# Optimization experiments

Measured on AMD Instinct MI355X. Metric: run time of the kernel, lower is better.

## Reference

```python
import jax, jax.numpy as jnp
import numpy as np

N_PEP, N_MHC, N_TCR = 20000, 5000, 100000
EMB, HID = 128, 256
E_PM, E_MT = 200000, 400000
B = 50000


def setup_inputs() -> dict:
    key = jax.random.key(0)
    ks = jax.random.split(key, 30)
    f32 = jnp.float32

    def w(k, shape, fan_in):
        # torch Linear default: U(-1/sqrt(fan_in), 1/sqrt(fan_in))
        lim = 1.0 / np.sqrt(fan_in)
        return jax.random.uniform(k, shape, dtype=f32, minval=-lim, maxval=lim)

    inp = {
        # embedding tables (learned params)
        "emb_pep": jax.random.normal(ks[0], (N_PEP, EMB), dtype=f32),
        "emb_mhc": jax.random.normal(ks[1], (N_MHC, EMB), dtype=f32),
        "emb_tcr": jax.random.normal(ks[2], (N_TCR, EMB), dtype=f32),
        # edge lists (src=edge_index[0], dst=edge_index[1])
        "src_pm": jax.random.randint(ks[3], (E_PM,), 0, N_PEP, dtype=jnp.int32),
        "dst_pm": jax.random.randint(ks[4], (E_PM,), 0, N_MHC, dtype=jnp.int32),
        "src_mt": jax.random.randint(ks[5], (E_MT,), 0, N_MHC, dtype=jnp.int32),
        "dst_mt": jax.random.randint(ks[6], (E_MT,), 0, N_TCR, dtype=jnp.int32),
        # triplet pack indices
        "pack_pep": jax.random.randint(ks[7], (B,), 0, N_PEP, dtype=jnp.int32),
        "pack_mhc": jax.random.randint(ks[8], (B,), 0, N_MHC, dtype=jnp.int32),
        "pack_tcr": jax.random.randint(ks[9], (B,), 0, N_TCR, dtype=jnp.int32),
        # SAGEConv params: Wl (aggregated neighbors, with bias), Wr (root, no bias)
        # layer 1: pep->mhc (src 128, dst 128); mhc->tcr (src 128, dst 128)
        "l1_pm_Wl": w(ks[10], (HID, EMB), EMB), "l1_pm_bl": w(ks[11], (HID,), EMB),
        "l1_pm_Wr": w(ks[12], (HID, EMB), EMB),
        "l1_mt_Wl": w(ks[13], (HID, EMB), EMB), "l1_mt_bl": w(ks[14], (HID,), EMB),
        "l1_mt_Wr": w(ks[15], (HID, EMB), EMB),
        # layer 2: pep->mhc (src 128, dst 256); mhc->tcr (src 256, dst 256)
        "l2_pm_Wl": w(ks[16], (HID, EMB), EMB), "l2_pm_bl": w(ks[17], (HID,), EMB),
        "l2_pm_Wr": w(ks[18], (HID, HID), HID),
        "l2_mt_Wl": w(ks[19], (HID, HID), HID), "l2_mt_bl": w(ks[20], (HID,), HID),
        "l2_mt_Wr": w(ks[21], (HID, HID), HID),
        # proj_pep and head MLP
        "proj_W": w(ks[22], (HID, EMB), EMB), "proj_b": w(ks[23], (HID,), EMB),
        "head_W1": w(ks[24], (HID, 3 * HID), 3 * HID), "head_b1": w(ks[25], (HID,), 3 * HID),
        "head_W2": w(ks[26], (1, HID), HID), "head_b2": w(ks[27], (1,), HID),
    }
    return inp


def _sage(x_src, x_dst, src, dst, Wl, bl, Wr, n_dst):
    # SAGEConv(mean): lin_l(mean_{j in N(i)} x_src[j]) + lin_r(x_dst[i])
    msg = jax.ops.segment_sum(x_src[src], dst, num_segments=n_dst)  # [n_dst, d_src]
    cnt = jax.ops.segment_sum(jnp.ones((src.shape[0],), x_src.dtype), dst, num_segments=n_dst)
    mean = msg / jnp.maximum(cnt, 1.0)[:, None]
    return mean @ Wl.T + bl + x_dst @ Wr.T


def reference(emb_pep, emb_mhc, emb_tcr,
              src_pm, dst_pm, src_mt, dst_mt,
              pack_pep, pack_mhc, pack_tcr,
              l1_pm_Wl, l1_pm_bl, l1_pm_Wr, l1_mt_Wl, l1_mt_bl, l1_mt_Wr,
              l2_pm_Wl, l2_pm_bl, l2_pm_Wr, l2_mt_Wl, l2_mt_bl, l2_mt_Wr,
              proj_W, proj_b, head_W1, head_b1, head_W2, head_b2):
    relu = jax.nn.relu
    # layer 1 (HeteroConv reads all relations from the same input dict)
    mhc1 = relu(_sage(emb_pep, emb_mhc, src_pm, dst_pm, l1_pm_Wl, l1_pm_bl, l1_pm_Wr, N_MHC))
    tcr1 = relu(_sage(emb_mhc, emb_tcr, src_mt, dst_mt, l1_mt_Wl, l1_mt_bl, l1_mt_Wr, N_TCR))
    # layer 2 ('pep' is never a destination, so it keeps its embedding)
    mhc2 = relu(_sage(emb_pep, mhc1, src_pm, dst_pm, l2_pm_Wl, l2_pm_bl, l2_pm_Wr, N_MHC))
    tcr2 = relu(_sage(mhc1, tcr1, src_mt, dst_mt, l2_mt_Wl, l2_mt_bl, l2_mt_Wr, N_TCR))
    # projections + triplet gather (dropout disabled: inference)
    hp = (emb_pep @ proj_W.T + proj_b)[pack_pep]  # [B, HID]
    hm = mhc2[pack_mhc]
    ht = tcr2[pack_tcr]
    z = jnp.concatenate([hp, hm, ht], axis=-1)  # [B, 3*HID]
    hidden = relu(z @ head_W1.T + head_b1)
    logits = hidden @ head_W2.T + head_b2
    return logits.squeeze(-1)
```

## Files before the change

### kernel.cpp

```cpp
#include <hip/hip_runtime.h>

constexpr int NPEP = 20000, NMHC = 5000, NTCR = 100000;
constexpr int EPM = 200000, EMT = 400000, BB = 50000;
constexpr int MAXU = 50000;

typedef __attribute__((ext_vector_type(8))) short bf16x8;
typedef __attribute__((ext_vector_type(4))) float f32x4;

__device__ inline ushort f2bf(float x) {
    union { float f; unsigned u; } v; v.f = x;
    unsigned r = (v.u + 0x7FFF + ((v.u >> 16) & 1)) >> 16;
    return (ushort)r;
}
__device__ inline float bf2f(ushort b) {
    union { unsigned u; float f; } t; t.u = ((unsigned)b) << 16; return t.f;
}
__device__ inline void bf2x2(unsigned u, float& a, float& b) {
    union { unsigned x; float f; } t1, t2;
    t1.x = u << 16; t2.x = u & 0xffff0000u;
    a = t1.f; b = t2.f;
}
__device__ inline ushort4 f4bf(float4 v) {
    return make_ushort4(f2bf(v.x), f2bf(v.y), f2bf(v.z), f2bf(v.w));
}

constexpr int RS  = 40;
constexpr int RS1 = 136;
constexpr int RS2 = 264;

template <int K, bool HASB, bool AF32>
__device__ void out_tile(ushort* Als, ushort* Wls, int tid, int bx, int by, int M,
                         const void* __restrict__ Av, const ushort* __restrict__ W,
                         const float* __restrict__ bias, ushort* __restrict__ out) {
    const int m0 = bx * 128, n0 = by * 128;
    const int lane = tid & 63, w = tid >> 6;
    const int wm = w >> 1, wn = w & 1;
    const int m16 = lane & 15, q = lane >> 4;

    f32x4 acc[4][4] = {};

    for (int k0 = 0; k0 < K; k0 += 32) {
        bf16x8 a_st[2], w_st[2];
#pragma unroll
        for (int r = 0; r < 2; r++) {
            int chunk = tid + r * 256;
            int row = chunk >> 2, off = (chunk & 3) * 8;
            int ga = min(m0 + row, M - 1);
            if constexpr (AF32) {
                const float* Af = (const float*)Av;
                float4 f0 = *(const float4*)(Af + (size_t)ga * K + k0 + off);
                float4 f1 = *(const float4*)(Af + (size_t)ga * K + k0 + off + 4);
                ushort4 u0 = f4bf(f0), u1 = f4bf(f1);
                bf16x8 av;
                av[0] = (short)u0.x; av[1] = (short)u0.y; av[2] = (short)u0.z; av[3] = (short)u0.w;
                av[4] = (short)u1.x; av[5] = (short)u1.y; av[6] = (short)u1.z; av[7] = (short)u1.w;
                a_st[r] = av;
            } else {
                a_st[r] = *(const bf16x8*)((const ushort*)Av + (size_t)ga * K + k0 + off);
            }
            w_st[r] = *(const bf16x8*)(W + (size_t)(n0 + row) * K + k0 + off);
        }
        __syncthreads();
#pragma unroll
        for (int r = 0; r < 2; r++) {
            int chunk = tid + r * 256;
            int row = chunk >> 2, off = (chunk & 3) * 8;
            *(bf16x8*)(&Als[row * RS + off]) = a_st[r];
            *(bf16x8*)(&Wls[row * RS + off]) = w_st[r];
        }
        __syncthreads();
        bf16x8 af[4], bf[4];
#pragma unroll
        for (int t = 0; t < 4; t++) {
            af[t] = *(const bf16x8*)(&Als[(wm * 64 + t * 16 + m16) * RS + q * 8]);
            bf[t] = *(const bf16x8*)(&Wls[(wn * 64 + t * 16 + m16) * RS + q * 8]);
        }
#pragma unroll
        for (int mt = 0; mt < 4; mt++)
#pragma unroll
            for (int nt = 0; nt < 4; nt++)
                acc[mt][nt] = __builtin_amdgcn_mfma_f32_16x16x32_bf16(af[mt], bf[nt], acc[mt][nt], 0, 0, 0);
    }

#pragma unroll
    for (int mt = 0; mt < 4; mt++) {
#pragma unroll
        for (int i = 0; i < 4; i++) {
            int row = m0 + wm * 64 + mt * 16 + q * 4 + i;
            if (row >= M) continue;
#pragma unroll
            for (int nt = 0; nt < 4; nt++) {
                int col = n0 + wn * 64 + nt * 16 + m16;
                float v = acc[mt][nt][i];
                if (HASB) v += bias[col];
                out[(size_t)row * 256 + col] = f2bf(v);
            }
        }
    }
}

__global__ __launch_bounds__(256) void prep_kernel(
    int* __restrict__ ibz,
    const float4* __restrict__ Wr1f, ushort4* __restrict__ Wr1_b,
    const float4* __restrict__ Wr2f, ushort4* __restrict__ Wr2_b,
    const float* __restrict__ head_W1, ushort4* __restrict__ W1b_b, ushort4* __restrict__ W1c_b,
    const float* __restrict__ l1_pm_Wl, const float* __restrict__ l1_pm_Wr,
    const float* __restrict__ l1_mt_Wl, ushort* __restrict__ Wcat1_b,
    const float* __restrict__ l2_pm_Wl, const float* __restrict__ l2_pm_Wr,
    const float* __restrict__ l2_mt_Wl, ushort* __restrict__ Wcat2_b,
    const float4* __restrict__ emb_mhc, ushort* __restrict__ Acat1,
    const float* __restrict__ proj_W, const float* __restrict__ proj_b,
    ushort* __restrict__ Wcomp_b, float* __restrict__ bp) {
    __shared__ float red[128];
    const int b = blockIdx.x, tid = threadIdx.x;
    if (b < 303) {
        int i = b * 256 + tid;
        if (i < 77500) ((int4*)ibz)[i] = make_int4(0, 0, 0, 0);
    } else if (b < 335) {
        int i = (b - 303) * 256 + tid;
        if (i < 8192) Wr1_b[i] = f4bf(Wr1f[i]);
    } else if (b < 399) {
        int i = (b - 335) * 256 + tid;
        if (i < 16384) Wr2_b[i] = f4bf(Wr2f[i]);
    } else if (b < 463) {
        int i = (b - 399) * 256 + tid;
        if (i < 16384) {
            int n = i >> 6, k4 = (i & 63) * 4;
            W1b_b[i] = f4bf(*(const float4*)(head_W1 + (size_t)n * 768 + 256 + k4));
        }
    } else if (b < 527) {
        int i = (b - 463) * 256 + tid;
        if (i < 16384) {
            int n = i >> 6, k4 = (i & 63) * 4;
            W1c_b[i] = f4bf(*(const float4*)(head_W1 + (size_t)n * 768 + 512 + k4));
        }
    } else if (b < 1039) {
        int idx = (b - 527) * 256 + tid;
        if (idx < 131072) {
            int r = idx >> 8, k = idx & 255;
            float v;
            if (r < 256) v = (k < 128) ? l1_pm_Wl[r * 128 + k] : l1_pm_Wr[r * 128 + (k - 128)];
            else         v = (k < 128) ? 0.f : l1_mt_Wl[(r - 256) * 128 + (k - 128)];
            Wcat1_b[idx] = f2bf(v);
        }
    } else if (b < 1807) {
        int idx = (b - 1039) * 256 + tid;
        if (idx < 196608) {
            int r = idx / 384, k = idx - r * 384;
            float v;
            if (r < 256) v = (k < 128) ? l2_pm_Wl[r * 128 + k] : l2_pm_Wr[r * 256 + (k - 128)];
            else         v = (k < 128) ? 0.f : l2_mt_Wl[(r - 256) * 256 + (k - 128)];
            Wcat2_b[idx] = f2bf(v);
        }
    } else if (b < 2432) {
        int i4 = (b - 1807) * 256 + tid;
        if (i4 < 160000) {
            int r = i4 >> 5, c4 = (i4 & 31) * 4;
            *(ushort4*)(Acat1 + (size_t)r * 256 + 128 + c4) = f4bf(emb_mhc[i4]);
        }
    } else {
        int i = b - 2432;
        const float* w1row = head_W1 + (size_t)i * 768;
        if (tid < 128) {
            float acc = 0.f;
            for (int k = 0; k < 256; k++) acc += w1row[k] * proj_W[k * 128 + tid];
            Wcomp_b[i * 128 + tid] = f2bf(acc);
            red[tid] = w1row[2 * tid] * proj_b[2 * tid] + w1row[2 * tid + 1] * proj_b[2 * tid + 1];
        }
        __syncthreads();
        if (tid < 64) { red[tid] += red[tid + 64]; }
        __syncthreads();
        if (tid < 32) { red[tid] += red[tid + 32]; }
        __syncthreads();
        if (tid == 0) {
            float s = 0.f;
            for (int j = 0; j < 32; j++) s += red[j];
            bp[i] = s;
        }
    }
}

__global__ void hist2_kernel(const int* __restrict__ dst_pm, const int* __restrict__ dst_mt,
                             const int* __restrict__ pack_tcr,
                             int* __restrict__ deg_pm, int* __restrict__ deg_mt,
                             int* __restrict__ mark) {
    int t = blockIdx.x * blockDim.x + threadIdx.x;
    if (t < EPM) atomicAdd(&deg_pm[dst_pm[t]], 1);
    else if (t < EPM + EMT) atomicAdd(&deg_mt[dst_mt[t - EPM]], 1);
    else if (t < EPM + EMT + BB) mark[pack_tcr[t - EPM - EMT]] = 1;
}

__global__ __launch_bounds__(256) void blocksum2_kernel(const int* __restrict__ deg_pm,
                                                        const int* __restrict__ deg_mt,
                                                        const int* __restrict__ mark,
                                                        int* __restrict__ bsum_pm,
                                                        int* __restrict__ bsum_mt,
                                                        int* __restrict__ bsum_mk) {
    __shared__ int red[256];
    const int tid = threadIdx.x;
    const int* deg; int n, bi; int* bsum;
    if (blockIdx.x < 5) { deg = deg_pm; n = NMHC; bi = blockIdx.x; bsum = bsum_pm; }
    else if (blockIdx.x < 103) { deg = deg_mt; n = NTCR; bi = blockIdx.x - 5; bsum = bsum_mt; }
    else { deg = mark; n = NTCR; bi = blockIdx.x - 103; bsum = bsum_mk; }
    const int base = bi * 1024;
    int s = 0;
#pragma unroll
    for (int j = 0; j < 4; j++) {
        int i = base + tid + j * 256;
        if (i < n) s += deg[i];
    }
    red[tid] = s;
    __syncthreads();
    for (int off = 128; off > 0; off >>= 1) {
        if (tid < off) red[tid] += red[tid + off];
        __syncthreads();
    }
    if (tid == 0) bsum[bi] = red[0];
}

__global__ __launch_bounds__(128) void scanb2_kernel(int* __restrict__ bsum_pm,
                                                     int* __restrict__ bsum_mt,
                                                     int* __restrict__ bsum_mk) {
    __shared__ int s[128];
    const int tid = threadIdx.x;
    int* bsum = (blockIdx.x == 0) ? bsum_pm : ((blockIdx.x == 1) ? bsum_mt : bsum_mk);
    const int nb = (blockIdx.x == 0) ? 5 : 98;
    int v = (tid < nb) ? bsum[tid] : 0;
    s[tid] = v;
    __syncthreads();
    for (int off = 1; off < 128; off <<= 1) {
        int t = (tid >= off) ? s[tid - off] : 0;
        __syncthreads();
        s[tid] += t;
        __syncthreads();
    }
    if (tid < nb) bsum[tid] = (tid > 0) ? s[tid - 1] : 0;
    if (tid == 0) bsum[nb] = s[nb - 1];
}

__global__ __launch_bounds__(256) void emit2_kernel(const int* __restrict__ deg_pm,
                                                    const int* __restrict__ deg_mt,
                                                    const int* __restrict__ mark,
                                                    const int* __restrict__ bsum_pm,
                                                    const int* __restrict__ bsum_mt,
                                                    const int* __restrict__ bsum_mk,
                                                    int* __restrict__ rp_pm,
                                                    int* __restrict__ rp_mt,
                                                    int* __restrict__ list,
                                                    int* __restrict__ inv) {
    __shared__ int tsum[256];
    const int tid = threadIdx.x;
    const int* deg; const int* bsum; int* rp; int n, nb, bi, mode;
    if (blockIdx.x < 5) { deg = deg_pm; bsum = bsum_pm; rp = rp_pm; n = NMHC; nb = 5; bi = blockIdx.x; mode = 0; }
    else if (blockIdx.x < 103) { deg = deg_mt; bsum = bsum_mt; rp = rp_mt; n = NTCR; nb = 98; bi = blockIdx.x - 5; mode = 0; }
    else { deg = mark; bsum = bsum_mk; rp = nullptr; n = NTCR; nb = 98; bi = blockIdx.x - 103; mode = 1; }
    const int i0 = bi * 1024 + tid * 4;
    int4 v = make_int4(0, 0, 0, 0);
    if (i0 + 3 < n) v = *(const int4*)(deg + i0);
    else if (i0 < n) {
        int t[4] = {0, 0, 0, 0};
        for (int j = 0; j < 4 && i0 + j < n; j++) t[j] = deg[i0 + j];
        v = make_int4(t[0], t[1], t[2], t[3]);
    }
    tsum[tid] = v.x + v.y + v.z + v.w;
    __syncthreads();
    for (int off = 1; off < 256; off <<= 1) {
        int t = (tid >= off) ? tsum[tid - off] : 0;
        __syncthreads();
        tsum[tid] += t;
        __syncthreads();
    }
    int ex = ((tid > 0) ? tsum[tid - 1] : 0) + bsum[bi];
    if (mode == 0) {
        if (i0 + 3 < n) {
            int r1 = ex + v.x, r2 = r1 + v.y, r3 = r2 + v.z;
            *(int4*)(rp + i0) = make_int4(ex, r1, r2, r3);
        } else if (i0 < n) {
            int r = ex;
            int vv[4] = {v.x, v.y, v.z, v.w};
            for (int j = 0; j < 4 && i0 + j < n; j++) { rp[i0 + j] = r; r += vv[j]; }
        }
        if (bi == 0 && tid == 0) rp[n] = bsum[nb];
    } else {
        int p = ex;
        int vv[4] = {v.x, v.y, v.z, v.w};
#pragma unroll
        for (int j = 0; j < 4; j++) {
            if (i0 + j < n && vv[j]) { list[p] = i0 + j; inv[i0 + j] = p; p++; }
        }
    }
}

__global__ void fill2_kernel(const int* __restrict__ src_pm, const int* __restrict__ dst_pm,
                             const int* __restrict__ src_mt, const int* __restrict__ dst_mt,
                             const int* __restrict__ rp_pm, int* __restrict__ cur_pm, int* __restrict__ csr_pm,
                             const int* __restrict__ rp_mt, int* __restrict__ cur_mt, int* __restrict__ csr_mt) {
    int t = blockIdx.x * blockDim.x + threadIdx.x;
    if (t < EPM) {
        int d = dst_pm[t];
        int pos = atomicAdd(&cur_pm[d], 1);
        csr_pm[rp_pm[d] + pos] = src_pm[t];
    } else if (t < EPM + EMT) {
        int t2 = t - EPM;
        int d = dst_mt[t2];
        int pos = atomicAdd(&cur_mt[d], 1);
        csr_mt[rp_mt[d] + pos] = src_mt[t2];
    }
}

__global__ __launch_bounds__(256, 2) void gph_kernel(
    const int* __restrict__ rp, const int* __restrict__ csr_src,
    const float* __restrict__ X, ushort* __restrict__ A1, ushort* __restrict__ A2,
    const float* __restrict__ emb_pep, const ushort* __restrict__ Wcomp,
    const float* __restrict__ bp, ushort* __restrict__ Hp,
    const int* __restrict__ pack_tcr, const int* __restrict__ inv, int* __restrict__ pt_c) {
    __shared__ ushort Als[128 * RS];
    __shared__ ushort Wls[128 * RS];
    const int tid = threadIdx.x;
    const int b = blockIdx.x;
    if (b < 625) {
        const int r = b * 8 + (tid >> 5);
        const int lane = tid & 31;
        if (r >= NMHC) return;
        const int e0 = rp[r], e1 = rp[r + 1];
        float4 s = make_float4(0.f, 0.f, 0.f, 0.f);
        for (int e = e0; e < e1; e++) {
            const int sidx = csr_src[e];
            float4 v = ((const float4*)(X + (long)sidx * 128))[lane];
            s.x += v.x; s.y += v.y; s.z += v.z; s.w += v.w;
        }
        float sc = 1.f / fmaxf((float)(e1 - e0), 1.f);
        ushort4 o = make_ushort4(f2bf(s.x * sc), f2bf(s.y * sc), f2bf(s.z * sc), f2bf(s.w * sc));
        *(ushort4*)(A1 + (size_t)r * 256 + lane * 4) = o;
        *(ushort4*)(A2 + (size_t)r * 384 + lane * 4) = o;
    } else if (b < 939) {
        int v = b - 625;
        out_tile<128, true, true>(Als, Wls, tid, v % 157, v / 157, NPEP,
                                  emb_pep, Wcomp, bp, Hp);
    } else {
        int i = (b - 939) * 256 + tid;
        if (i < BB) pt_c[i] = inv[pack_tcr[i]];
    }
}

template <int K, int NB0, bool RELU0, bool G2>
__global__ __launch_bounds__(256, 2) void mfma_fused_kernel(
    int M, const ushort* __restrict__ A, const ushort* __restrict__ W,
    const float* __restrict__ bias,
    ushort* __restrict__ out0, int s0, ushort* __restrict__ out1) {
    __shared__ ushort Als[128 * RS];
    __shared__ ushort Wls[128 * RS];
    const int tid = threadIdx.x;
    const int m0 = blockIdx.x * 128, n0 = blockIdx.y * 128;
    const int lane = tid & 63, w = tid >> 6;
    const int wm = w >> 1, wn = w & 1;
    const int m16 = lane & 15, q = lane >> 4;

    f32x4 acc[4][4] = {};

    for (int k0 = 0; k0 < K; k0 += 32) {
        bf16x8 a_st[2], w_st[2];
#pragma unroll
        for (int r = 0; r < 2; r++) {
            int chunk = tid + r * 256;
            int row = chunk >> 2, off = (chunk & 3) * 8;
            int ga = min(m0 + row, M - 1);
            a_st[r] = *(const bf16x8*)(A + (size_t)ga * K + k0 + off);
            w_st[r] = *(const bf16x8*)(W + (size_t)(n0 + row) * K + k0 + off);
        }
        __syncthreads();
#pragma unroll
        for (int r = 0; r < 2; r++) {
            int chunk = tid + r * 256;
            int row = chunk >> 2, off = (chunk & 3) * 8;
            *(bf16x8*)(&Als[row * RS + off]) = a_st[r];
            *(bf16x8*)(&Wls[row * RS + off]) = w_st[r];
        }
        __syncthreads();
        bf16x8 af[4], bf[4];
#pragma unroll
        for (int t = 0; t < 4; t++) {
            af[t] = *(const bf16x8*)(&Als[(wm * 64 + t * 16 + m16) * RS + q * 8]);
            bf[t] = *(const bf16x8*)(&Wls[(wn * 64 + t * 16 + m16) * RS + q * 8]);
        }
#pragma unroll
        for (int mt = 0; mt < 4; mt++)
#pragma unroll
            for (int nt = 0; nt < 4; nt++)
                acc[mt][nt] = __builtin_amdgcn_mfma_f32_16x16x32_bf16(af[mt], bf[nt], acc[mt][nt], 0, 0, 0);
    }

    const bool g1 = G2 && ((int)blockIdx.y >= NB0);
#pragma unroll
    for (int mt = 0; mt < 4; mt++) {
#pragma unroll
        for (int i = 0; i < 4; i++) {
            int row = m0 + wm * 64 + mt * 16 + q * 4 + i;
            if (row >= M) continue;
#pragma unroll
            for (int nt = 0; nt < 4; nt++) {
                int col = n0 + wn * 64 + nt * 16 + m16;
                float v = acc[mt][nt][i];
                if (!g1) {
                    v += bias[col];
                    if (RELU0) v = fmaxf(v, 0.f);
                    out0[(size_t)row * s0 + col] = f2bf(v);
                } else {
                    out1[(size_t)row * 256 + (col - NB0 * 128)] = f2bf(v);
                }
            }
        }
    }
}

__global__ __launch_bounds__(256, 3) void tcrhm_kernel(
    const int* __restrict__ nrowsp, const int* __restrict__ list,
    const int* __restrict__ rp, const int* __restrict__ csr_src,
    const ushort* __restrict__ Z1, const ushort* __restrict__ Z2,
    const float* __restrict__ emb_tcr,
    const ushort* __restrict__ Wr1, const ushort* __restrict__ Wr2,
    const ushort* __restrict__ W1c,
    const float* __restrict__ bl1, const float* __restrict__ bl2,
    ushort* __restrict__ Ht_c,
    const ushort* __restrict__ mhc2, const ushort* __restrict__ W1b,
    ushort* __restrict__ Hm) {
    union SM {
        struct { ushort B[32 * RS2]; ushort A1[32 * RS2]; ushort A2[32 * RS2]; } t;
        struct { ushort Als[128 * RS]; ushort Wls[128 * RS]; } g;
    };
    __shared__ SM sm;
    const int tid = threadIdx.x;

    if (blockIdx.x >= 1563) {
        int v = blockIdx.x - 1563;
        out_tile<256, false, false>(sm.g.Als, sm.g.Wls, tid, v % 40, v / 40, NMHC,
                                    mhc2, W1b, nullptr, Hm);
        return;
    }

    const int M = nrowsp[0];
    const int m0 = blockIdx.x * 32;
    if (m0 >= M) return;
    const int lane = tid & 63, w = tid >> 6;
    const int m16 = lane & 15, q = lane >> 4;

#pragma unroll
    for (int r = 0; r < 4; r++) {
        int chunk = tid + r * 256;
        int row = chunk >> 5, c4 = (chunk & 31) * 4;
        int grow = list[min(m0 + row, M - 1)];
        float4 v = *(const float4*)(emb_tcr + (size_t)grow * 128 + c4);
        *(ushort4*)(&sm.t.B[row * RS1 + c4]) = f4bf(v);
    }

    {
        const int g = tid >> 5, gl = tid & 31;
        for (int rr = g; rr < 32; rr += 8) {
            int cr = min(m0 + rr, M - 1);
            int orig = list[cr];
            int e0 = rp[orig], e1 = rp[orig + 1];
            int deg = e1 - e0;
            float s1[8] = {}, s2[8] = {};
            int sidx_l = (gl < deg) ? csr_src[e0 + gl] : 0;
            int dn = min(deg, 32);
            for (int e = 0; e < dn; e++) {
                int sidx = __shfl(sidx_l, e, 32);
                uint4 u1 = *(const uint4*)(Z1 + (size_t)sidx * 256 + gl * 8);
                uint4 u2 = *(const uint4*)(Z2 + (size_t)sidx * 256 + gl * 8);
                float x, y;
                bf2x2(u1.x, x, y); s1[0] += x; s1[1] += y;
                bf2x2(u1.y, x, y); s1[2] += x; s1[3] += y;
                bf2x2(u1.z, x, y); s1[4] += x; s1[5] += y;
                bf2x2(u1.w, x, y); s1[6] += x; s1[7] += y;
                bf2x2(u2.x, x, y); s2[0] += x; s2[1] += y;
                bf2x2(u2.y, x, y); s2[2] += x; s2[3] += y;
                bf2x2(u2.z, x, y); s2[4] += x; s2[5] += y;
                bf2x2(u2.w, x, y); s2[6] += x; s2[7] += y;
            }
            for (int e = e0 + 32; e < e1; e++) {
                int sidx = csr_src[e];
                uint4 u1 = *(const uint4*)(Z1 + (size_t)sidx * 256 + gl * 8);
                uint4 u2 = *(const uint4*)(Z2 + (size_t)sidx * 256 + gl * 8);
                float x, y;
                bf2x2(u1.x, x, y); s1[0] += x; s1[1] += y;
                bf2x2(u1.y, x, y); s1[2] += x; s1[3] += y;
                bf2x2(u1.z, x, y); s1[4] += x; s1[5] += y;
                bf2x2(u1.w, x, y); s1[6] += x; s1[7] += y;
                bf2x2(u2.x, x, y); s2[0] += x; s2[1] += y;
                bf2x2(u2.y, x, y); s2[2] += x; s2[3] += y;
                bf2x2(u2.z, x, y); s2[4] += x; s2[5] += y;
                bf2x2(u2.w, x, y); s2[6] += x; s2[7] += y;
            }
            float es = 1.f / fmaxf((float)deg, 1.f);
            uint4 w1, w2;
            w1.x = (unsigned)f2bf(s1[0] * es) | ((unsigned)f2bf(s1[1] * es) << 16);
            w1.y = (unsigned)f2bf(s1[2] * es) | ((unsigned)f2bf(s1[3] * es) << 16);
            w1.z = (unsigned)f2bf(s1[4] * es) | ((unsigned)f2bf(s1[5] * es) << 16);
            w1.w = (unsigned)f2bf(s1[6] * es) | ((unsigned)f2bf(s1[7] * es) << 16);
            w2.x = (unsigned)f2bf(s2[0] * es) | ((unsigned)f2bf(s2[1] * es) << 16);
            w2.y = (unsigned)f2bf(s2[2] * es) | ((unsigned)f2bf(s2[3] * es) << 16);
            w2.z = (unsigned)f2bf(s2[4] * es) | ((unsigned)f2bf(s2[5] * es) << 16);
            w2.w = (unsigned)f2bf(s2[6] * es) | ((unsigned)f2bf(s2[7] * es) << 16);
            *(uint4*)(&sm.t.A1[rr * RS2 + gl * 8]) = w1;
            *(uint4*)(&sm.t.A2[rr * RS2 + gl * 8]) = w2;
        }
    }
    __syncthreads();

    {
        f32x4 acc[2][4] = {};
        for (int k0 = 0; k0 < 128; k0 += 32) {
            bf16x8 af[2], bf[4];
#pragma unroll
            for (int t = 0; t < 2; t++)
                af[t] = *(const bf16x8*)(&sm.t.B[(t * 16 + m16) * RS1 + k0 + q * 8]);
#pragma unroll
            for (int t = 0; t < 4; t++)
                bf[t] = *(const bf16x8*)(Wr1 + (size_t)(w * 64 + t * 16 + m16) * 128 + k0 + q * 8);
#pragma unroll
            for (int mt = 0; mt < 2; mt++)
#pragma unroll
                for (int nt = 0; nt < 4; nt++)
                    acc[mt][nt] = __builtin_amdgcn_mfma_f32_16x16x32_bf16(af[mt], bf[nt], acc[mt][nt], 0, 0, 0);
        }
        __syncthreads();
#pragma unroll
        for (int mt = 0; mt < 2; mt++)
#pragma unroll
            for (int i = 0; i < 4; i++) {
                int lr = mt * 16 + q * 4 + i;
#pragma unroll
                for (int nt = 0; nt < 4; nt++) {
                    int col = w * 64 + nt * 16 + m16;
                    float v = acc[mt][nt][i] + bl1[col] + bf2f(sm.t.A1[lr * RS2 + col]);
                    sm.t.B[lr * RS2 + col] = f2bf(fmaxf(v, 0.f));
                }
            }
    }
    __syncthreads();

    {
        f32x4 acc[2][4] = {};
        for (int k0 = 0; k0 < 256; k0 += 32) {
            bf16x8 af[2], bf[4];
#pragma unroll
            for (int t = 0; t < 2; t++)
                af[t] = *(const bf16x8*)(&sm.t.B[(t * 16 + m16) * RS2 + k0 + q * 8]);
#pragma unroll
            for (int t = 0; t < 4; t++)
                bf[t] = *(const bf16x8*)(Wr2 + (size_t)(w * 64 + t * 16 + m16) * 256 + k0 + q * 8);
#pragma unroll
            for (int mt = 0; mt < 2; mt++)
#pragma unroll
                for (int nt = 0; nt < 4; nt++)
                    acc[mt][nt] = __builtin_amdgcn_mfma_f32_16x16x32_bf16(af[mt], bf[nt], acc[mt][nt], 0, 0, 0);
        }
        __syncthreads();
#pragma unroll
        for (int mt = 0; mt < 2; mt++)
#pragma unroll
            for (int i = 0; i < 4; i++) {
                int lr = mt * 16 + q * 4 + i;
#pragma unroll
                for (int nt = 0; nt < 4; nt++) {
                    int col = w * 64 + nt * 16 + m16;
                    float v = acc[mt][nt][i] + bl2[col] + bf2f(sm.t.A2[lr * RS2 + col]);
                    sm.t.B[lr * RS2 + col] = f2bf(fmaxf(v, 0.f));
                }
            }
    }
    __syncthreads();

    {
        f32x4 acc[2][4] = {};
        for (int k0 = 0; k0 < 256; k0 += 32) {
            bf16x8 af[2], bf[4];
#pragma unroll
            for (int t = 0; t < 2; t++)
                af[t] = *(const bf16x8*)(&sm.t.B[(t * 16 + m16) * RS2 + k0 + q * 8]);
#pragma unroll
            for (int t = 0; t < 4; t++)
                bf[t] = *(const bf16x8*)(W1c + (size_t)(w * 64 + t * 16 + m16) * 256 + k0 + q * 8);
#pragma unroll
            for (int mt = 0; mt < 2; mt++)
#pragma unroll
                for (int nt = 0; nt < 4; nt++)
                    acc[mt][nt] = __builtin_amdgcn_mfma_f32_16x16x32_bf16(af[mt], bf[nt], acc[mt][nt], 0, 0, 0);
        }
        __syncthreads();
#pragma unroll
        for (int mt = 0; mt < 2; mt++)
#pragma unroll
            for (int i = 0; i < 4; i++) {
                int lr = mt * 16 + q * 4 + i;
#pragma unroll
                for (int nt = 0; nt < 4; nt++) {
                    int col = w * 64 + nt * 16 + m16;
                    sm.t.B[lr * RS2 + col] = f2bf(acc[mt][nt][i]);
                }
            }
    }
    __syncthreads();

#pragma unroll
    for (int r = 0; r < 4; r++) {
        int chunk = tid + r * 256;
        int row = chunk >> 5, c8 = (chunk & 31) * 8;
        if (m0 + row < M)
            *(uint4*)(Ht_c + (size_t)(m0 + row) * 256 + c8) = *(const uint4*)(&sm.t.B[row * RS2 + c8]);
    }
}

__global__ __launch_bounds__(256) void combine_kernel(
    const ushort* __restrict__ Hp, const ushort* __restrict__ Hm, const ushort* __restrict__ Ht,
    const int* __restrict__ pp, const int* __restrict__ pm, const int* __restrict__ pt_c,
    const float* __restrict__ b1, const float* __restrict__ W2, const float* __restrict__ b2,
    float* __restrict__ out) {
    const int tid = threadIdx.x;
    const int lane = tid & 63, w = tid >> 6;
    const int c = lane * 4;
    const float4 b1v = *(const float4*)(b1 + c);
    const float4 w2v = *(const float4*)(W2 + c);
    const float b2v = b2[0];
    const int base = blockIdx.x * 32 + w * 8;
#pragma unroll
    for (int t = 0; t < 8; t++) {
        int i = base + t;
        if (i >= BB) return;
        int ra = pp[i], rb = pm[i], rc = pt_c[i];
        ushort4 ua = *(const ushort4*)(Hp + (size_t)ra * 256 + c);
        ushort4 ub = *(const ushort4*)(Hm + (size_t)rb * 256 + c);
        ushort4 uc = *(const ushort4*)(Ht + (size_t)rc * 256 + c);
        float h0 = fmaxf(bf2f(ua.x) + bf2f(ub.x) + bf2f(uc.x) + b1v.x, 0.f);
        float h1 = fmaxf(bf2f(ua.y) + bf2f(ub.y) + bf2f(uc.y) + b1v.y, 0.f);
        float h2 = fmaxf(bf2f(ua.z) + bf2f(ub.z) + bf2f(uc.z) + b1v.z, 0.f);
        float h3 = fmaxf(bf2f(ua.w) + bf2f(ub.w) + bf2f(uc.w) + b1v.w, 0.f);
        float p = h0 * w2v.x + h1 * w2v.y + h2 * w2v.z + h3 * w2v.w;
#pragma unroll
        for (int off = 32; off > 0; off >>= 1) p += __shfl_down(p, off);
        if (lane == 0) out[i] = p + b2v;
    }
}

extern "C" void kernel_launch(void* const* d_in, const int* in_sizes, int n_in,
                              void* d_out, int out_size, void* d_ws, size_t ws_size,
                              hipStream_t stream) {
    const float* emb_pep = (const float*)d_in[0];
    const float* emb_mhc = (const float*)d_in[1];
    const float* emb_tcr = (const float*)d_in[2];
    const int* src_pm = (const int*)d_in[3];
    const int* dst_pm = (const int*)d_in[4];
    const int* src_mt = (const int*)d_in[5];
    const int* dst_mt = (const int*)d_in[6];
    const int* pack_pep = (const int*)d_in[7];
    const int* pack_mhc = (const int*)d_in[8];
    const int* pack_tcr = (const int*)d_in[9];
    const float* l1_pm_Wl = (const float*)d_in[10];
    const float* l1_pm_bl = (const float*)d_in[11];
    const float* l1_pm_Wr = (const float*)d_in[12];
    const float* l1_mt_Wl = (const float*)d_in[13];
    const float* l1_mt_bl = (const float*)d_in[14];
    const float* l1_mt_Wr = (const float*)d_in[15];
    const float* l2_pm_Wl = (const float*)d_in[16];
    const float* l2_pm_bl = (const float*)d_in[17];
    const float* l2_pm_Wr = (const float*)d_in[18];
    const float* l2_mt_Wl = (const float*)d_in[19];
    const float* l2_mt_bl = (const float*)d_in[20];
    const float* l2_mt_Wr = (const float*)d_in[21];
    const float* proj_W = (const float*)d_in[22];
    const float* proj_b = (const float*)d_in[23];
    const float* head_W1 = (const float*)d_in[24];
    const float* head_b1 = (const float*)d_in[25];
    const float* head_W2 = (const float*)d_in[26];
    const float* head_b2 = (const float*)d_in[27];
    float* out = (float*)d_out;

    int* ib = (int*)d_ws;
    int* deg_pm = ib;
    int* cur_pm = ib + 5000;
    int* deg_mt = ib + 10000;
    int* cur_mt = ib + 110000;
    int* mark   = ib + 210000;
    int* rp_pm  = ib + 310000;
    int* rp_mt  = ib + 315008;
    int* csr_pm = ib + 415016;
    int* csr_mt = ib + 615016;
    int* bsum_pm = ib + 1015016;
    int* bsum_mt = ib + 1015176;
    int* bsum_mk = ib + 1015336;
    int* list    = ib + 1015496;
    int* inv     = ib + 1065544;
    int* pt_c    = ib + 1165544;

    float* f = (float*)(ib + 1215592);
    float* bp = f;

    ushort* u = (ushort*)(f + 256);
    ushort* Wcat1_b = u;
    ushort* Wcat2_b = u + 131072;
    ushort* W1b_b   = u + 327680;
    ushort* W1c_b   = u + 393216;
    ushort* Wcomp_b = u + 458752;
    ushort* Wr1_b   = u + 491520;
    ushort* Wr2_b   = u + 524288;
    ushort* Acat1   = u + 589824;
    ushort* Acat2   = u + 1869824;
    ushort* Zb1     = u + 3789824;
    ushort* Zb2     = u + 5069824;
    ushort* mhc2_b  = u + 6349824;
    ushort* Hp_b    = u + 7629824;
    ushort* Hm_b    = u + 12749824;
    ushort* Ht_c    = u + 14029824;

    prep_kernel<<<2688, 256, 0, stream>>>(
        ib,
        (const float4*)l1_mt_Wr, (ushort4*)Wr1_b,
        (const float4*)l2_mt_Wr, (ushort4*)Wr2_b,
        head_W1, (ushort4*)W1b_b, (ushort4*)W1c_b,
        l1_pm_Wl, l1_pm_Wr, l1_mt_Wl, Wcat1_b,
        l2_pm_Wl, l2_pm_Wr, l2_mt_Wl, Wcat2_b,
        (const float4*)emb_mhc, Acat1,
        proj_W, proj_b, Wcomp_b, bp);

    hist2_kernel<<<(EPM + EMT + BB + 255) / 256, 256, 0, stream>>>(
        dst_pm, dst_mt, pack_tcr, deg_pm, deg_mt, mark);
    blocksum2_kernel<<<201, 256, 0, stream>>>(deg_pm, deg_mt, mark, bsum_pm, bsum_mt, bsum_mk);
    scanb2_kernel<<<3, 128, 0, stream>>>(bsum_pm, bsum_mt, bsum_mk);
    emit2_kernel<<<201, 256, 0, stream>>>(deg_pm, deg_mt, mark, bsum_pm, bsum_mt, bsum_mk,
                                          rp_pm, rp_mt, list, inv);
    fill2_kernel<<<(EPM + EMT + 255) / 256, 256, 0, stream>>>(
        src_pm, dst_pm, src_mt, dst_mt, rp_pm, cur_pm, csr_pm, rp_mt, cur_mt, csr_mt);

    gph_kernel<<<1135, 256, 0, stream>>>(
        rp_pm, csr_pm, emb_pep, Acat1, Acat2,
        emb_pep, Wcomp_b, bp, Hp_b,
        pack_tcr, inv, pt_c);

    mfma_fused_kernel<256, 2, true, true><<<dim3((NMHC + 127) / 128, 4), 256, 0, stream>>>(
        NMHC, Acat1, Wcat1_b, l1_pm_bl, Acat2 + 128, 384, Zb1);
    mfma_fused_kernel<384, 2, true, true><<<dim3((NMHC + 127) / 128, 4), 256, 0, stream>>>(
        NMHC, Acat2, Wcat2_b, l2_pm_bl, mhc2_b, 256, Zb2);

    tcrhm_kernel<<<1563 + 80, 256, 0, stream>>>(
        bsum_mk + 98, list, rp_mt, csr_mt, Zb1, Zb2, emb_tcr,
        Wr1_b, Wr2_b, W1c_b, l1_mt_bl, l2_mt_bl, Ht_c,
        mhc2_b, W1b_b, Hm_b);

    combine_kernel<<<(BB + 31) / 32, 256, 0, stream>>>(
        Hp_b, Hm_b, Ht_c, pack_pep, pack_mhc, pt_c,
        head_b1, head_W2, head_b2, out);
}
```

Before: 385.1 us.

## Merge histogram into prep, drop scan kernel, split Hp GEMM, reduce tcrhm LDS

Several changes land together. The histogram pass is folded into the prep kernel, with zeroing moved to a memset. The separate block-sum scan kernel is removed: each emit block now reduces the preceding block sums itself and writes the row count. The Hp projection GEMM moves out of the gather kernel and is split across the two MHC GEMM launches, which may balance work across them. tcrhm now gathers Z1 and Z2 in two sequential passes into a single shared buffer, cutting LDS so more blocks fit per CU (launch bounds raised to 4). The trade is that the edge lists are read twice.

Result: no change. 391.9 us (+1.8%).

```diff
diff --git a/kernel.cpp b/kernel.cpp
--- a/kernel.cpp
+++ b/kernel.cpp
@@ -27,6 +27,73 @@
 constexpr int RS  = 40;
 constexpr int RS1 = 136;
 constexpr int RS2 = 264;
+
+template <int K, int NB0>
+__device__ void fused_tile(ushort* Als, ushort* Wls, int tid, int bx, int by, int M,
+                           const ushort* __restrict__ A, const ushort* __restrict__ W,
+                           const float* __restrict__ bias,
+                           ushort* __restrict__ out0, int s0, ushort* __restrict__ out1) {
+    const int m0 = bx * 128, n0 = by * 128;
+    const int lane = tid & 63, w = tid >> 6;
+    const int wm = w >> 1, wn = w & 1;
+    const int m16 = lane & 15, q = lane >> 4;
+
+    f32x4 acc[4][4] = {};
+
+    for (int k0 = 0; k0 < K; k0 += 32) {
+        bf16x8 a_st[2], w_st[2];
+#pragma unroll
+        for (int r = 0; r < 2; r++) {
+            int chunk = tid + r * 256;
+            int row = chunk >> 2, off = (chunk & 3) * 8;
+            int ga = min(m0 + row, M - 1);
+            a_st[r] = *(const bf16x8*)(A + (size_t)ga * K + k0 + off);
+            w_st[r] = *(const bf16x8*)(W + (size_t)(n0 + row) * K + k0 + off);
+        }
+        __syncthreads();
+#pragma unroll
+        for (int r = 0; r < 2; r++) {
+            int chunk = tid + r * 256;
+            int row = chunk >> 2, off = (chunk & 3) * 8;
+            *(bf16x8*)(&Als[row * RS + off]) = a_st[r];
+            *(bf16x8*)(&Wls[row * RS + off]) = w_st[r];
+        }
+        __syncthreads();
+        bf16x8 af[4], bf[4];
+#pragma unroll
+        for (int t = 0; t < 4; t++) {
+            af[t] = *(const bf16x8*)(&Als[(wm * 64 + t * 16 + m16) * RS + q * 8]);
+            bf[t] = *(const bf16x8*)(&Wls[(wn * 64 + t * 16 + m16) * RS + q * 8]);
+        }
+#pragma unroll
+        for (int mt = 0; mt < 4; mt++)
+#pragma unroll
+            for (int nt = 0; nt < 4; nt++)
+                acc[mt][nt] = __builtin_amdgcn_mfma_f32_16x16x32_bf16(af[mt], bf[nt], acc[mt][nt], 0, 0, 0);
+    }
+
+    const bool g1 = (by >= NB0);
+#pragma unroll
+    for (int mt = 0; mt < 4; mt++) {
+#pragma unroll
+        for (int i = 0; i < 4; i++) {
+            int row = m0 + wm * 64 + mt * 16 + q * 4 + i;
+            if (row >= M) continue;
+#pragma unroll
+            for (int nt = 0; nt < 4; nt++) {
+                int col = n0 + wn * 64 + nt * 16 + m16;
+                float v = acc[mt][nt][i];
+                if (!g1) {
+                    v += bias[col];
+                    v = fmaxf(v, 0.f);
+                    out0[(size_t)row * s0 + col] = f2bf(v);
+                } else {
+                    out1[(size_t)row * 256 + (col - NB0 * 128)] = f2bf(v);
+                }
+            }
+        }
+    }
+}
 
 template <int K, bool HASB, bool AF32>
 __device__ void out_tile(ushort* Als, ushort* Wls, int tid, int bx, int by, int M,
@@ -99,8 +166,43 @@
     }
 }
 
-__global__ __launch_bounds__(256) void prep_kernel(
-    int* __restrict__ ibz,
+__device__ void gather_pass(ushort* A, const int* __restrict__ list,
+                            const int* __restrict__ rp, const int* __restrict__ csr_src,
+                            const ushort* __restrict__ Z, int m0, int M, int tid) {
+    const int g = tid >> 5, gl = tid & 31;
+    for (int rr = g; rr < 32; rr += 8) {
+        int cr = min(m0 + rr, M - 1);
+        int orig = list[cr];
+        int e0 = rp[orig], e1 = rp[orig + 1];
+        int deg = e1 - e0;
+        float s[8] = {};
+        for (int eb = e0; eb < e1; eb += 32) {
+            int dc = min(32, e1 - eb);
+            int sidx_l = (gl < dc) ? csr_src[eb + gl] : 0;
+            for (int e = 0; e < dc; e++) {
+                int sidx = __shfl(sidx_l, e, 32);
+                uint4 u = *(const uint4*)(Z + (size_t)sidx * 256 + gl * 8);
+                float x, y;
+                bf2x2(u.x, x, y); s[0] += x; s[1] += y;
+                bf2x2(u.y, x, y); s[2] += x; s[3] += y;
+                bf2x2(u.z, x, y); s[4] += x; s[5] += y;
+                bf2x2(u.w, x, y); s[6] += x; s[7] += y;
+            }
+        }
+        float es = 1.f / fmaxf((float)deg, 1.f);
+        uint4 w;
+        w.x = (unsigned)f2bf(s[0] * es) | ((unsigned)f2bf(s[1] * es) << 16);
+        w.y = (unsigned)f2bf(s[2] * es) | ((unsigned)f2bf(s[3] * es) << 16);
+        w.z = (unsigned)f2bf(s[4] * es) | ((unsigned)f2bf(s[5] * es) << 16);
+        w.w = (unsigned)f2bf(s[6] * es) | ((unsigned)f2bf(s[7] * es) << 16);
+        *(uint4*)(&A[rr * RS2 + gl * 8]) = w;
+    }
+}
+
+__global__ __launch_bounds__(256) void preph_kernel(
+    const int* __restrict__ dst_pm, const int* __restrict__ dst_mt,
+    const int* __restrict__ pack_tcr,
+    int* __restrict__ deg_pm, int* __restrict__ deg_mt, int* __restrict__ mark,
     const float4* __restrict__ Wr1f, ushort4* __restrict__ Wr1_b,
     const float4* __restrict__ Wr2f, ushort4* __restrict__ Wr2_b,
     const float* __restrict__ head_W1, ushort4* __restrict__ W1b_b, ushort4* __restrict__ W1c_b,
@@ -113,29 +215,31 @@
     ushort* __restrict__ Wcomp_b, float* __restrict__ bp) {
     __shared__ float red[128];
     const int b = blockIdx.x, tid = threadIdx.x;
-    if (b < 303) {
-        int i = b * 256 + tid;
-        if (i < 77500) ((int4*)ibz)[i] = make_int4(0, 0, 0, 0);
-    } else if (b < 335) {
-        int i = (b - 303) * 256 + tid;
+    if (b < 2540) {
+        int t = b * 256 + tid;
+        if (t < EPM) atomicAdd(&deg_pm[dst_pm[t]], 1);
+        else if (t < EPM + EMT) atomicAdd(&deg_mt[dst_mt[t - EPM]], 1);
+        else if (t < EPM + EMT + BB) mark[pack_tcr[t - EPM - EMT]] = 1;
+    } else if (b < 2572) {
+        int i = (b - 2540) * 256 + tid;
         if (i < 8192) Wr1_b[i] = f4bf(Wr1f[i]);
-    } else if (b < 399) {
-        int i = (b - 335) * 256 + tid;
+    } else if (b < 2636) {
+        int i = (b - 2572) * 256 + tid;
         if (i < 16384) Wr2_b[i] = f4bf(Wr2f[i]);
-    } else if (b < 463) {
-        int i = (b - 399) * 256 + tid;
+    } else if (b < 2700) {
+        int i = (b - 2636) * 256 + tid;
         if (i < 16384) {
             int n = i >> 6, k4 = (i & 63) * 4;
             W1b_b[i] = f4bf(*(const float4*)(head_W1 + (size_t)n * 768 + 256 + k4));
         }
-    } else if (b < 527) {
-        int i = (b - 463) * 256 + tid;
+    } else if (b < 2764) {
+        int i = (b - 2700) * 256 + tid;
         if (i < 16384) {
             int n = i >> 6, k4 = (i & 63) * 4;
             W1c_b[i] = f4bf(*(const float4*)(head_W1 + (size_t)n * 768 + 512 + k4));
         }
-    } else if (b < 1039) {
-        int idx = (b - 527) * 256 + tid;
+    } else if (b < 3276) {
+        int idx = (b - 2764) * 256 + tid;
         if (idx < 131072) {
             int r = idx >> 8, k = idx & 255;
             float v;
@@ -143,8 +247,8 @@
             else         v = (k < 128) ? 0.f : l1_mt_Wl[(r - 256) * 128 + (k - 128)];
             Wcat1_b[idx] = f2bf(v);
         }
-    } else if (b < 1807) {
-        int idx = (b - 1039) * 256 + tid;
+    } else if (b < 4044) {
+        int idx = (b - 3276) * 256 + tid;
         if (idx < 196608) {
             int r = idx / 384, k = idx - r * 384;
             float v;
@@ -152,14 +256,14 @@
             else         v = (k < 128) ? 0.f : l2_mt_Wl[(r - 256) * 256 + (k - 128)];
             Wcat2_b[idx] = f2bf(v);
         }
-    } else if (b < 2432) {
-        int i4 = (b - 1807) * 256 + tid;
+    } else if (b < 4669) {
+        int i4 = (b - 4044) * 256 + tid;
         if (i4 < 160000) {
             int r = i4 >> 5, c4 = (i4 & 31) * 4;
             *(ushort4*)(Acat1 + (size_t)r * 256 + 128 + c4) = f4bf(emb_mhc[i4]);
         }
     } else {
-        int i = b - 2432;
+        int i = b - 4669;
         const float* w1row = head_W1 + (size_t)i * 768;
         if (tid < 128) {
             float acc = 0.f;
@@ -178,16 +282,6 @@
             bp[i] = s;
         }
     }
-}
-
-__global__ void hist2_kernel(const int* __restrict__ dst_pm, const int* __restrict__ dst_mt,
-                             const int* __restrict__ pack_tcr,
-                             int* __restrict__ deg_pm, int* __restrict__ deg_mt,
-                             int* __restrict__ mark) {
-    int t = blockIdx.x * blockDim.x + threadIdx.x;
-    if (t < EPM) atomicAdd(&deg_pm[dst_pm[t]], 1);
-    else if (t < EPM + EMT) atomicAdd(&deg_mt[dst_mt[t - EPM]], 1);
-    else if (t < EPM + EMT + BB) mark[pack_tcr[t - EPM - EMT]] = 1;
 }
 
 __global__ __launch_bounds__(256) void blocksum2_kernel(const int* __restrict__ deg_pm,
@@ -218,26 +312,6 @@
     if (tid == 0) bsum[bi] = red[0];
 }
 
-__global__ __launch_bounds__(128) void scanb2_kernel(int* __restrict__ bsum_pm,
-                                                     int* __restrict__ bsum_mt,
-                                                     int* __restrict__ bsum_mk) {
-    __shared__ int s[128];
-    const int tid = threadIdx.x;
-    int* bsum = (blockIdx.x == 0) ? bsum_pm : ((blockIdx.x == 1) ? bsum_mt : bsum_mk);
-    const int nb = (blockIdx.x == 0) ? 5 : 98;
-    int v = (tid < nb) ? bsum[tid] : 0;
-    s[tid] = v;
-    __syncthreads();
-    for (int off = 1; off < 128; off <<= 1) {
-        int t = (tid >= off) ? s[tid - off] : 0;
-        __syncthreads();
-        s[tid] += t;
-        __syncthreads();
-    }
-    if (tid < nb) bsum[tid] = (tid > 0) ? s[tid - 1] : 0;
-    if (tid == 0) bsum[nb] = s[nb - 1];
-}
-
 __global__ __launch_bounds__(256) void emit2_kernel(const int* __restrict__ deg_pm,
                                                     const int* __restrict__ deg_mt,
                                                     const int* __restrict__ mark,
@@ -247,13 +321,22 @@
                                                     int* __restrict__ rp_pm,
                                                     int* __restrict__ rp_mt,
                                                     int* __restrict__ list,
-                                                    int* __restrict__ inv) {
+                                                    int* __restrict__ inv,
+                                                    int* __restrict__ nrows) {
     __shared__ int tsum[256];
     const int tid = threadIdx.x;
     const int* deg; const int* bsum; int* rp; int n, nb, bi, mode;
     if (blockIdx.x < 5) { deg = deg_pm; bsum = bsum_pm; rp = rp_pm; n = NMHC; nb = 5; bi = blockIdx.x; mode = 0; }
     else if (blockIdx.x < 103) { deg = deg_mt; bsum = bsum_mt; rp = rp_mt; n = NTCR; nb = 98; bi = blockIdx.x - 5; mode = 0; }
     else { deg = mark; bsum = bsum_mk; rp = nullptr; n = NTCR; nb = 98; bi = blockIdx.x - 103; mode = 1; }
+    tsum[tid] = (tid < bi) ? bsum[tid] : 0;
+    __syncthreads();
+    for (int off = 128; off > 0; off >>= 1) {
+        if (tid < off) tsum[tid] += tsum[tid + off];
+        __syncthreads();
+    }
+    const int base = tsum[0];
+    __syncthreads();
     const int i0 = bi * 1024 + tid * 4;
     int4 v = make_int4(0, 0, 0, 0);
     if (i0 + 3 < n) v = *(const int4*)(deg + i0);
@@ -270,7 +353,7 @@
         tsum[tid] += t;
         __syncthreads();
     }
-    int ex = ((tid > 0) ? tsum[tid - 1] : 0) + bsum[bi];
+    int ex = ((tid > 0) ? tsum[tid - 1] : 0) + base;
     if (mode == 0) {
         if (i0 + 3 < n) {
             int r1 = ex + v.x, r2 = r1 + v.y, r3 = r2 + v.z;
@@ -280,7 +363,7 @@
             int vv[4] = {v.x, v.y, v.z, v.w};
             for (int j = 0; j < 4 && i0 + j < n; j++) { rp[i0 + j] = r; r += vv[j]; }
         }
-        if (bi == 0 && tid == 0) rp[n] = bsum[nb];
+        if (bi == nb - 1 && tid == 255) rp[n] = base + tsum[255];
     } else {
         int p = ex;
         int vv[4] = {v.x, v.y, v.z, v.w};
@@ -288,6 +371,7 @@
         for (int j = 0; j < 4; j++) {
             if (i0 + j < n && vv[j]) { list[p] = i0 + j; inv[i0 + j] = p; p++; }
         }
+        if (bi == nb - 1 && tid == 255) nrows[0] = base + tsum[255];
     }
 }
 
@@ -308,14 +392,10 @@
     }
 }
 
-__global__ __launch_bounds__(256, 2) void gph_kernel(
+__global__ __launch_bounds__(256) void gph_kernel(
     const int* __restrict__ rp, const int* __restrict__ csr_src,
     const float* __restrict__ X, ushort* __restrict__ A1, ushort* __restrict__ A2,
-    const float* __restrict__ emb_pep, const ushort* __restrict__ Wcomp,
-    const float* __restrict__ bp, ushort* __restrict__ Hp,
     const int* __restrict__ pack_tcr, const int* __restrict__ inv, int* __restrict__ pt_c) {
-    __shared__ ushort Als[128 * RS];
-    __shared__ ushort Wls[128 * RS];
     const int tid = threadIdx.x;
     const int b = blockIdx.x;
     if (b < 625) {
@@ -324,96 +404,43 @@
         if (r >= NMHC) return;
         const int e0 = rp[r], e1 = rp[r + 1];
         float4 s = make_float4(0.f, 0.f, 0.f, 0.f);
-        for (int e = e0; e < e1; e++) {
-            const int sidx = csr_src[e];
-            float4 v = ((const float4*)(X + (long)sidx * 128))[lane];
-            s.x += v.x; s.y += v.y; s.z += v.z; s.w += v.w;
+        for (int eb = e0; eb < e1; eb += 32) {
+            int dc = min(32, e1 - eb);
+            int sidx_l = (lane < dc) ? csr_src[eb + lane] : 0;
+            for (int e = 0; e < dc; e++) {
+                int sidx = __shfl(sidx_l, e, 32);
+                float4 v = ((const float4*)(X + (long)sidx * 128))[lane];
+                s.x += v.x; s.y += v.y; s.z += v.z; s.w += v.w;
+            }
         }
         float sc = 1.f / fmaxf((float)(e1 - e0), 1.f);
         ushort4 o = make_ushort4(f2bf(s.x * sc), f2bf(s.y * sc), f2bf(s.z * sc), f2bf(s.w * sc));
         *(ushort4*)(A1 + (size_t)r * 256 + lane * 4) = o;
         *(ushort4*)(A2 + (size_t)r * 384 + lane * 4) = o;
-    } else if (b < 939) {
-        int v = b - 625;
-        out_tile<128, true, true>(Als, Wls, tid, v % 157, v / 157, NPEP,
-                                  emb_pep, Wcomp, bp, Hp);
     } else {
-        int i = (b - 939) * 256 + tid;
+        int i = (b - 625) * 256 + tid;
         if (i < BB) pt_c[i] = inv[pack_tcr[i]];
     }
 }
 
-template <int K, int NB0, bool RELU0, bool G2>
-__global__ __launch_bounds__(256, 2) void mfma_fused_kernel(
+template <int K>
+__global__ __launch_bounds__(256, 2) void fusedhp_kernel(
     int M, const ushort* __restrict__ A, const ushort* __restrict__ W,
     const float* __restrict__ bias,
-    ushort* __restrict__ out0, int s0, ushort* __restrict__ out1) {
+    ushort* __restrict__ out0, int s0, ushort* __restrict__ out1,
+    int hpBy, const float* __restrict__ emb_pep, const ushort* __restrict__ Wcomp,
+    const float* __restrict__ bp, ushort* __restrict__ Hp) {
     __shared__ ushort Als[128 * RS];
     __shared__ ushort Wls[128 * RS];
     const int tid = threadIdx.x;
-    const int m0 = blockIdx.x * 128, n0 = blockIdx.y * 128;
-    const int lane = tid & 63, w = tid >> 6;
-    const int wm = w >> 1, wn = w & 1;
-    const int m16 = lane & 15, q = lane >> 4;
-
-    f32x4 acc[4][4] = {};
-
-    for (int k0 = 0; k0 < K; k0 += 32) {
-        bf16x8 a_st[2], w_st[2];
-#pragma unroll
-        for (int r = 0; r < 2; r++) {
-            int chunk = tid + r * 256;
-            int row = chunk >> 2, off = (chunk & 3) * 8;
-            int ga = min(m0 + row, M - 1);
-            a_st[r] = *(const bf16x8*)(A + (size_t)ga * K + k0 + off);
-            w_st[r] = *(const bf16x8*)(W + (size_t)(n0 + row) * K + k0 + off);
-        }
-        __syncthreads();
-#pragma unroll
-        for (int r = 0; r < 2; r++) {
-            int chunk = tid + r * 256;
-            int row = chunk >> 2, off = (chunk & 3) * 8;
-            *(bf16x8*)(&Als[row * RS + off]) = a_st[r];
-            *(bf16x8*)(&Wls[row * RS + off]) = w_st[r];
-        }
-        __syncthreads();
-        bf16x8 af[4], bf[4];
-#pragma unroll
-        for (int t = 0; t < 4; t++) {
-            af[t] = *(const bf16x8*)(&Als[(wm * 64 + t * 16 + m16) * RS + q * 8]);
-            bf[t] = *(const bf16x8*)(&Wls[(wn * 64 + t * 16 + m16) * RS + q * 8]);
-        }
-#pragma unroll
-        for (int mt = 0; mt < 4; mt++)
-#pragma unroll
-            for (int nt = 0; nt < 4; nt++)
-                acc[mt][nt] = __builtin_amdgcn_mfma_f32_16x16x32_bf16(af[mt], bf[nt], acc[mt][nt], 0, 0, 0);
-    }
-
-    const bool g1 = G2 && ((int)blockIdx.y >= NB0);
-#pragma unroll
-    for (int mt = 0; mt < 4; mt++) {
-#pragma unroll
-        for (int i = 0; i < 4; i++) {
-            int row = m0 + wm * 64 + mt * 16 + q * 4 + i;
-            if (row >= M) continue;
-#pragma unroll
-            for (int nt = 0; nt < 4; nt++) {
-                int col = n0 + wn * 64 + nt * 16 + m16;
-                float v = acc[mt][nt][i];
-                if (!g1) {
-                    v += bias[col];
-                    if (RELU0) v = fmaxf(v, 0.f);
-                    out0[(size_t)row * s0 + col] = f2bf(v);
-                } else {
-                    out1[(size_t)row * 256 + (col - NB0 * 128)] = f2bf(v);
-                }
-            }
-        }
-    }
-}
-
-__global__ __launch_bounds__(256, 3) void tcrhm_kernel(
+    const int b = blockIdx.x;
+    if (b < 160)
+        fused_tile<K, 2>(Als, Wls, tid, b % 40, b / 40, M, A, W, bias, out0, s0, out1);
+    else
+        out_tile<128, true, true>(Als, Wls, tid, b - 160, hpBy, NPEP, emb_pep, Wcomp, bp, Hp);
+}
+
+__global__ __launch_bounds__(256, 4) void tcrhm_kernel(
     const int* __restrict__ nrowsp, const int* __restrict__ list,
     const int* __restrict__ rp, const int* __restrict__ csr_src,
     const ushort* __restrict__ Z1, const ushort* __restrict__ Z2,
@@ -425,7 +452,7 @@
     const ushort* __restrict__ mhc2, const ushort* __restrict__ W1b,
     ushort* __restrict__ Hm) {
     union SM {
-        struct { ushort B[32 * RS2]; ushort A1[32 * RS2]; ushort A2[32 * RS2]; } t;
+        struct { ushort B[32 * RS2]; ushort A[32 * RS2]; } t;
         struct { ushort Als[128 * RS]; ushort Wls[128 * RS]; } g;
     };
     __shared__ SM sm;
@@ -453,58 +480,7 @@
         *(ushort4*)(&sm.t.B[row * RS1 + c4]) = f4bf(v);
     }
 
-    {
-        const int g = tid >> 5, gl = tid & 31;
-        for (int rr = g; rr < 32; rr += 8) {
-            int cr = min(m0 + rr, M - 1);
-            int orig = list[cr];
-            int e0 = rp[orig], e1 = rp[orig + 1];
-            int deg = e1 - e0;
-            float s1[8] = {}, s2[8] = {};
-            int sidx_l = (gl < deg) ? csr_src[e0 + gl] : 0;
-            int dn = min(deg, 32);
-            for (int e = 0; e < dn; e++) {
-                int sidx = __shfl(sidx_l, e, 32);
-                uint4 u1 = *(const uint4*)(Z1 + (size_t)sidx * 256 + gl * 8);
-                uint4 u2 = *(const uint4*)(Z2 + (size_t)sidx * 256 + gl * 8);
-                float x, y;
-                bf2x2(u1.x, x, y); s1[0] += x; s1[1] += y;
-                bf2x2(u1.y, x, y); s1[2] += x; s1[3] += y;
-                bf2x2(u1.z, x, y); s1[4] += x; s1[5] += y;
-                bf2x2(u1.w, x, y); s1[6] += x; s1[7] += y;
-                bf2x2(u2.x, x, y); s2[0] += x; s2[1] += y;
-                bf2x2(u2.y, x, y); s2[2] += x; s2[3] += y;
-                bf2x2(u2.z, x, y); s2[4] += x; s2[5] += y;
-                bf2x2(u2.w, x, y); s2[6] += x; s2[7] += y;
-            }
-            for (int e = e0 + 32; e < e1; e++) {
-                int sidx = csr_src[e];
-                uint4 u1 = *(const uint4*)(Z1 + (size_t)sidx * 256 + gl * 8);
-                uint4 u2 = *(const uint4*)(Z2 + (size_t)sidx * 256 + gl * 8);
-                float x, y;
-                bf2x2(u1.x, x, y); s1[0] += x; s1[1] += y;
-                bf2x2(u1.y, x, y); s1[2] += x; s1[3] += y;
-                bf2x2(u1.z, x, y); s1[4] += x; s1[5] += y;
-                bf2x2(u1.w, x, y); s1[6] += x; s1[7] += y;
-                bf2x2(u2.x, x, y); s2[0] += x; s2[1] += y;
-                bf2x2(u2.y, x, y); s2[2] += x; s2[3] += y;
-                bf2x2(u2.z, x, y); s2[4] += x; s2[5] += y;
-                bf2x2(u2.w, x, y); s2[6] += x; s2[7] += y;
-            }
-            float es = 1.f / fmaxf((float)deg, 1.f);
-            uint4 w1, w2;
-            w1.x = (unsigned)f2bf(s1[0] * es) | ((unsigned)f2bf(s1[1] * es) << 16);
-            w1.y = (unsigned)f2bf(s1[2] * es) | ((unsigned)f2bf(s1[3] * es) << 16);
-            w1.z = (unsigned)f2bf(s1[4] * es) | ((unsigned)f2bf(s1[5] * es) << 16);
-            w1.w = (unsigned)f2bf(s1[6] * es) | ((unsigned)f2bf(s1[7] * es) << 16);
-            w2.x = (unsigned)f2bf(s2[0] * es) | ((unsigned)f2bf(s2[1] * es) << 16);
-            w2.y = (unsigned)f2bf(s2[2] * es) | ((unsigned)f2bf(s2[3] * es) << 16);
-            w2.z = (unsigned)f2bf(s2[4] * es) | ((unsigned)f2bf(s2[5] * es) << 16);
-            w2.w = (unsigned)f2bf(s2[6] * es) | ((unsigned)f2bf(s2[7] * es) << 16);
-            *(uint4*)(&sm.t.A1[rr * RS2 + gl * 8]) = w1;
-            *(uint4*)(&sm.t.A2[rr * RS2 + gl * 8]) = w2;
-        }
-    }
+    gather_pass(sm.t.A, list, rp, csr_src, Z1, m0, M, tid);
     __syncthreads();
 
     {
@@ -532,11 +508,14 @@
 #pragma unroll
                 for (int nt = 0; nt < 4; nt++) {
                     int col = w * 64 + nt * 16 + m16;
-                    float v = acc[mt][nt][i] + bl1[col] + bf2f(sm.t.A1[lr * RS2 + col]);
+                    float v = acc[mt][nt][i] + bl1[col] + bf2f(sm.t.A[lr * RS2 + col]);
                     sm.t.B[lr * RS2 + col] = f2bf(fmaxf(v, 0.f));
                 }
             }
     }
+    __syncthreads();
+
+    gather_pass(sm.t.A, list, rp, csr_src, Z2, m0, M, tid);
     __syncthreads();
 
     {
@@ -564,7 +543,7 @@
 #pragma unroll
                 for (int nt = 0; nt < 4; nt++) {
                     int col = w * 64 + nt * 16 + m16;
-                    float v = acc[mt][nt][i] + bl2[col] + bf2f(sm.t.A2[lr * RS2 + col]);
+                    float v = acc[mt][nt][i] + bl2[col] + bf2f(sm.t.A[lr * RS2 + col]);
                     sm.t.B[lr * RS2 + col] = f2bf(fmaxf(v, 0.f));
                 }
             }
@@ -688,11 +667,12 @@
     int* bsum_pm = ib + 1015016;
     int* bsum_mt = ib + 1015176;
     int* bsum_mk = ib + 1015336;
-    int* list    = ib + 1015496;
-    int* inv     = ib + 1065544;
-    int* pt_c    = ib + 1165544;
-
-    float* f = (float*)(ib + 1215592);
+    int* nrows   = ib + 1015496;
+    int* list    = ib + 1015504;
+    int* inv     = ib + 1065552;
+    int* pt_c    = ib + 1165552;
+
+    float* f = (float*)(ib + 1215600);
     float* bp = f;
 
     ushort* u = (ushort*)(f + 256);
@@ -712,8 +692,10 @@
     ushort* Hm_b    = u + 12749824;
     ushort* Ht_c    = u + 14029824;
 
-    prep_kernel<<<2688, 256, 0, stream>>>(
-        ib,
+    hipMemsetAsync(ib, 0, 310000 * sizeof(int), stream);
+
+    preph_kernel<<<4925, 256, 0, stream>>>(
+        dst_pm, dst_mt, pack_tcr, deg_pm, deg_mt, mark,
         (const float4*)l1_mt_Wr, (ushort4*)Wr1_b,
         (const float4*)l2_mt_Wr, (ushort4*)Wr2_b,
         head_W1, (ushort4*)W1b_b, (ushort4*)W1c_b,
@@ -722,27 +704,24 @@
         (const float4*)emb_mhc, Acat1,
         proj_W, proj_b, Wcomp_b, bp);
 
-    hist2_kernel<<<(EPM + EMT + BB + 255) / 256, 256, 0, stream>>>(
-        dst_pm, dst_mt, pack_tcr, deg_pm, deg_mt, mark);
     blocksum2_kernel<<<201, 256, 0, stream>>>(deg_pm, deg_mt, mark, bsum_pm, bsum_mt, bsum_mk);
-    scanb2_kernel<<<3, 128, 0, stream>>>(bsum_pm, bsum_mt, bsum_mk);
     emit2_kernel<<<201, 256, 0, stream>>>(deg_pm, deg_mt, mark, bsum_pm, bsum_mt, bsum_mk,
-                                          rp_pm, rp_mt, list, inv);
+                                          rp_pm, rp_mt, list, inv, nrows);
     fill2_kernel<<<(EPM + EMT + 255) / 256, 256, 0, stream>>>(
         src_pm, dst_pm, src_mt, dst_mt, rp_pm, cur_pm, csr_pm, rp_mt, cur_mt, csr_mt);
 
-    gph_kernel<<<1135, 256, 0, stream>>>(
-        rp_pm, csr_pm, emb_pep, Acat1, Acat2,
-        emb_pep, Wcomp_b, bp, Hp_b,
-        pack_tcr, inv, pt_c);
-
-    mfma_fused_kernel<256, 2, true, true><<<dim3((NMHC + 127) / 128, 4), 256, 0, stream>>>(
-        NMHC, Acat1, Wcat1_b, l1_pm_bl, Acat2 + 128, 384, Zb1);
-    mfma_fused_kernel<384, 2, true, true><<<dim3((NMHC + 127) / 128, 4), 256, 0, stream>>>(
-        NMHC, Acat2, Wcat2_b, l2_pm_bl, mhc2_b, 256, Zb2);
+    gph_kernel<<<821, 256, 0, stream>>>(
+        rp_pm, csr_pm, emb_pep, Acat1, Acat2, pack_tcr, inv, pt_c);
+
+    fusedhp_kernel<256><<<317, 256, 0, stream>>>(
+        NMHC, Acat1, Wcat1_b, l1_pm_bl, Acat2 + 128, 384, Zb1,
+        0, emb_pep, Wcomp_b, bp, Hp_b);
+    fusedhp_kernel<384><<<317, 256, 0, stream>>>(
+        NMHC, Acat2, Wcat2_b, l2_pm_bl, mhc2_b, 256, Zb2,
+        1, emb_pep, Wcomp_b, bp, Hp_b);
 
     tcrhm_kernel<<<1563 + 80, 256, 0, stream>>>(
-        bsum_mk + 98, list, rp_mt, csr_mt, Zb1, Zb2, emb_tcr,
+        nrows, list, rp_mt, csr_mt, Zb1, Zb2, emb_tcr,
         Wr1_b, Wr2_b, W1c_b, l1_mt_bl, l2_mt_bl, Ht_c,
         mhc2_b, W1b_b, Hm_b);
 
```
